# Performance work log

Hardware: AMD Instinct MI355X
Metric: run time of the kernel (lower is better)

The kernel has to match this reference:

```python
import jax, jax.numpy as jnp
import numpy as np

B, S, D, H = 4, 2048, 1024, 16
HD = D // H  # head_length = 64


def setup_inputs() -> dict:
    key = jax.random.key(0)
    ks = jax.random.split(key, 11)
    s = 1.0 / np.sqrt(D)
    return {
        "queries": jax.random.normal(ks[0], (B, S, D), jnp.float32),
        "keys": jax.random.normal(ks[1], (B, S, D), jnp.float32),
        "values": jax.random.normal(ks[2], (B, S, D), jnp.float32),
        "Wq": jax.random.normal(ks[3], (D, D), jnp.float32) * s,
        "bq": jnp.zeros((D,), jnp.float32),
        "Wk": jax.random.normal(ks[4], (D, D), jnp.float32) * s,
        "bk": jnp.zeros((D,), jnp.float32),
        "Wv": jax.random.normal(ks[5], (D, D), jnp.float32) * s,
        "bv": jnp.zeros((D,), jnp.float32),
        "Wo": jax.random.normal(ks[6], (D, D), jnp.float32) * s,
        "bo": jnp.zeros((D,), jnp.float32),
    }


def reference(queries, keys, values, Wq, bq, Wk, bk, Wv, bv, Wo, bo):
    # Linear projections (torch Linear: x @ W^T + b), split into heads -> [B, H, S, HD]
    def proj(x, W, b):
        return (x @ W.T + b).reshape(B, S, H, HD).transpose(0, 2, 1, 3)

    q = proj(queries, Wq, bq)
    k = proj(keys, Wk, bk)
    v = proj(values, Wv, bv)
    # Scaled dot-product attention, scale = 1/sqrt(head_length)
    scores = jnp.einsum("bhsd,bhtd->bhst", q, k) / jnp.sqrt(jnp.float32(HD))
    attn = jax.nn.softmax(scores, axis=-1)
    out = jnp.einsum("bhst,bhtd->bhsd", attn, v)  # [B, H, S, HD]
    out = out.transpose(0, 2, 1, 3).reshape(B, S, D)
    return out @ Wo.T + bo
```

## Files before the change

### kernel.cpp

```cpp
#include <hip/hip_runtime.h>
#include <stdint.h>
#include <stddef.h>

#define B_ 4
#define S_ 2048
#define D_ 1024
#define H_ 16
#define HD_ 64

#define QSCALE 0.18033688f

typedef __bf16 bf16;
typedef __bf16 bf16x8 __attribute__((ext_vector_type(8)));
typedef __bf16 bf16x4 __attribute__((ext_vector_type(4)));
typedef float f32x4 __attribute__((ext_vector_type(4)));
typedef float f32x16 __attribute__((ext_vector_type(16)));
typedef uint32_t u32x4 __attribute__((ext_vector_type(4)));

__device__ __forceinline__ f32x4 mfma16(bf16x8 a, bf16x8 b, f32x4 c) {
  return __builtin_amdgcn_mfma_f32_16x16x32_bf16(a, b, c, 0, 0, 0);
}
__device__ __forceinline__ f32x16 mfma32(bf16x8 a, bf16x8 b, f32x16 c) {
  return __builtin_amdgcn_mfma_f32_32x32x16_bf16(a, b, c, 0, 0, 0);
}

__device__ __forceinline__ float fexp2(float x) {
#if __has_builtin(__builtin_amdgcn_exp2f)
  return __builtin_amdgcn_exp2f(x);
#else
  return exp2f(x);
#endif
}

__device__ __forceinline__ void gload_lds16(const void* g, void* l) {
  __builtin_amdgcn_global_load_lds(
      (__attribute__((address_space(1))) uint32_t*)(uintptr_t)g,
      (__attribute__((address_space(3))) uint32_t*)l, 16, 0, 0);
}

__device__ __forceinline__ uint32_t cvt_pk(float lo, float hi) {
  uint32_t r;
  asm volatile("v_cvt_pk_bf16_f32 %0, %1, %2" : "=v"(r) : "v"(lo), "v"(hi));
  return r;
}

__device__ __forceinline__ void pl_swap(uint32_t& a, uint32_t& b) {
#if __has_builtin(__builtin_amdgcn_permlane32_swap)
  typedef int i32x2_t __attribute__((ext_vector_type(2)));
  i32x2_t r = __builtin_amdgcn_permlane32_swap((int)a, (int)b, false, false);
  a = (uint32_t)r[0];
  b = (uint32_t)r[1];
#else
  uint32_t pa_ = (uint32_t)__shfl_xor((int)a, 32);
  uint32_t pb_ = (uint32_t)__shfl_xor((int)b, 32);
  bool hi_ = (threadIdx.x & 32) != 0;
  uint32_t na = hi_ ? pb_ : a;
  uint32_t nb = hi_ ? b : pa_;
  a = na;
  b = nb;
#endif
}

__device__ __forceinline__ bf16x8 pack4(uint32_t a, uint32_t b, uint32_t c,
                                        uint32_t d) {
  u32x4 v = {a, b, c, d};
  return __builtin_bit_cast(bf16x8, v);
}

__global__ __launch_bounds__(256) void convert_w(
    const float* __restrict__ a, const float* __restrict__ b,
    const float* __restrict__ c, const float* __restrict__ d,
    bf16* __restrict__ out) {
  int i = (blockIdx.x * 256 + threadIdx.x) * 4;
  const float* srcs[4] = {a, b, c, d};
#pragma unroll
  for (int w = 0; w < 4; ++w) {
    f32x4 x = *(const f32x4*)(srcs[w] + i);
    bf16x4 v;
    v[0] = (bf16)x[0]; v[1] = (bf16)x[1]; v[2] = (bf16)x[2]; v[3] = (bf16)x[3];
    *(bf16x4*)(out + (size_t)w * (D_ * D_) + i) = v;
  }
}

__global__ __launch_bounds__(256) void convert_in(const float* __restrict__ in,
                                                  bf16* __restrict__ out) {
  const int n8 = (B_ * S_ * D_) / 8;
  for (int i = blockIdx.x * 256 + threadIdx.x; i < n8; i += gridDim.x * 256) {
    f32x4 x0 = *(const f32x4*)(in + (size_t)i * 8);
    f32x4 x1 = *(const f32x4*)(in + (size_t)i * 8 + 4);
    bf16x8 v;
    v[0] = (bf16)x0[0]; v[1] = (bf16)x0[1]; v[2] = (bf16)x0[2]; v[3] = (bf16)x0[3];
    v[4] = (bf16)x1[0]; v[5] = (bf16)x1[1]; v[6] = (bf16)x1[2]; v[7] = (bf16)x1[3];
    *(bf16x8*)(out + (size_t)i * 8) = v;
  }
}

template <int MODE>
__global__ __launch_bounds__(256, 2) void gemm_bf16(
    const bf16* __restrict__ A, const bf16* __restrict__ Wb,
    const float* __restrict__ bias, void* __restrict__ Out, float oscale) {
  __shared__ alignas(128) char lds[32768];
  const int tid = threadIdx.x;
  const int lane = tid & 63;
  const int wave = tid >> 6;
  const int m0 = blockIdx.x * 128;
  const int n0 = blockIdx.y * 128;
  const int wr = wave >> 1, wc = wave & 1;

  f32x4 acc[4][4] = {};

  for (int kt = 0; kt < 16; ++kt) {
    const int k0 = kt * 64;
#pragma unroll
    for (int j = 0; j < 4; ++j) {
      int slot = j * 256 + tid;
      int row = slot >> 3, kb = slot & 7;
      gload_lds16(A + (size_t)(m0 + row) * D_ + k0 + ((kb ^ (row & 7)) << 3),
                  lds + j * 4096 + wave * 1024);
    }
#pragma unroll
    for (int j = 0; j < 4; ++j) {
      int slot = j * 256 + tid;
      int row = slot >> 3, kb = slot & 7;
      gload_lds16(Wb + (size_t)(n0 + row) * D_ + k0 + ((kb ^ (row & 7)) << 3),
                  lds + 16384 + j * 4096 + wave * 1024);
    }
    __syncthreads();
#pragma unroll
    for (int ks = 0; ks < 2; ++ks) {
      bf16x8 af[4], bfr[4];
#pragma unroll
      for (int f = 0; f < 4; ++f) {
        int ar = wr * 64 + f * 16 + (lane & 15);
        af[f] = *(const bf16x8*)(lds + ar * 128 +
                                 (((ks * 4 + (lane >> 4)) ^ (ar & 7)) << 4));
        int br = wc * 64 + f * 16 + (lane & 15);
        bfr[f] = *(const bf16x8*)(lds + 16384 + br * 128 +
                                  (((ks * 4 + (lane >> 4)) ^ (br & 7)) << 4));
      }
#pragma unroll
      for (int i = 0; i < 4; ++i)
#pragma unroll
        for (int j = 0; j < 4; ++j)
          acc[i][j] = mfma16(af[i], bfr[j], acc[i][j]);
    }
    __syncthreads();
  }

#pragma unroll
  for (int j = 0; j < 4; ++j) {
    const int col = n0 + wc * 64 + j * 16 + (lane & 15);
    const float bv_ = bias[col];
    const int h = col >> 6, hd = col & 63;
#pragma unroll
    for (int i = 0; i < 4; ++i) {
      const int row0 = m0 + wr * 64 + i * 16 + ((lane >> 4) << 2);
      if (MODE == 2) {
        float* O = (float*)Out;
#pragma unroll
        for (int r = 0; r < 4; ++r)
          O[(size_t)(row0 + r) * D_ + col] = acc[i][j][r] + bv_;
      } else if (MODE == 0) {
        bf16* O = (bf16*)Out;
#pragma unroll
        for (int r = 0; r < 4; ++r) {
          int row = row0 + r;
          int b = row >> 11, s = row & (S_ - 1);
          O[(((size_t)(b * H_ + h) * S_ + s) << 6) + hd] =
              (bf16)((acc[i][j][r] + bv_) * oscale);
        }
      } else {
        bf16* O = (bf16*)Out;
        int b = row0 >> 11, s0 = row0 & (S_ - 1);
        bf16x4 pk;
#pragma unroll
        for (int r = 0; r < 4; ++r) pk[r] = (bf16)(acc[i][j][r] + bv_);
        *(bf16x4*)(O + ((size_t)(b * H_ + h) * HD_ + hd) * S_ + s0) = pk;
      }
    }
  }
}

__global__ __launch_bounds__(256, 2) void attn_kernel(
    const bf16* __restrict__ Qh, const bf16* __restrict__ Kh,
    const bf16* __restrict__ Vt, bf16* __restrict__ AO) {
  __shared__ alignas(128) char lds[2][16384];
  const int tid = threadIdx.x, lane = tid & 63, wave = tid >> 6;
  const int hi = lane >> 5, l31 = lane & 31;
  const int bid = blockIdx.x;
  const int bh = bid & 63;
  const int qb = bid >> 6;
  const int q0 = qb * 256 + wave * 64;
  const bf16* Qb = Qh + (size_t)bh * S_ * HD_;
  const bf16* Kb = Kh + (size_t)bh * S_ * HD_;
  const bf16* Vb = Vt + (size_t)bh * HD_ * S_;

  bf16x8 qf[2][4];
#pragma unroll
  for (int qg = 0; qg < 2; ++qg)
#pragma unroll
    for (int ks = 0; ks < 4; ++ks)
      qf[qg][ks] = *(const bf16x8*)(Qb + (size_t)(q0 + qg * 32 + l31) * HD_ +
                                    ks * 16 + hi * 8);

  const bf16* gs[4];
  int lo_[4], ginc[4];
#pragma unroll
  for (int j = 0; j < 4; ++j) {
    int f = j * 4 + wave;
    lo_[j] = f * 1024;
    if (f < 8) {
      gs[j] = Kb + (size_t)((f >> 2) * 32 + l31) * HD_ + (f & 3) * 16 + hi * 8;
      ginc[j] = 64 * HD_;
    } else {
      int g = f - 8;
      gs[j] = Vb + (size_t)((g & 1) * 32 + l31) * S_ + (g >> 1) * 16 + hi * 8;
      ginc[j] = 64;
    }
  }

  f32x16 oacc[2][2] = {};
  float dl[2] = {0.f, 0.f};

#pragma unroll
  for (int j = 0; j < 4; ++j) {
    gload_lds16(gs[j], &lds[0][lo_[j]]);
    gs[j] += ginc[j];
  }
  __syncthreads();

  for (int t = 0; t < 32; ++t) {
    const int cur = t & 1;
    if (t < 31) {
#pragma unroll
      for (int j = 0; j < 4; ++j) {
        gload_lds16(gs[j], &lds[cur ^ 1][lo_[j]]);
        gs[j] += ginc[j];
      }
    }
    const char* kbuf = lds[cur];
    const char* vbuf = lds[cur] + 8192;

    f32x16 s[2][2];
    s[0][0] = (f32x16){}; s[0][1] = (f32x16){};
    s[1][0] = (f32x16){}; s[1][1] = (f32x16){};
    __builtin_amdgcn_s_setprio(1);
#pragma unroll
    for (int kb = 0; kb < 2; ++kb)
#pragma unroll
      for (int ks = 0; ks < 4; ++ks) {
        bf16x8 kf = *(const bf16x8*)(kbuf + (kb * 4 + ks) * 1024 + lane * 16);
        s[kb][0] = mfma32(kf, qf[0][ks], s[kb][0]);
        s[kb][1] = mfma32(kf, qf[1][ks], s[kb][1]);
      }
    __builtin_amdgcn_s_setprio(0);

#pragma unroll
    for (int kb = 0; kb < 2; ++kb) {
      bf16x8 pa[2][2];
#pragma unroll
      for (int qg = 0; qg < 2; ++qg) {
        float e[16];
#pragma unroll
        for (int r = 0; r < 16; ++r) e[r] = fexp2(s[kb][qg][r]);
        {
          float a0 = e[0] + e[1], a1 = e[2] + e[3], a2 = e[4] + e[5],
                a3 = e[6] + e[7], a4 = e[8] + e[9], a5 = e[10] + e[11],
                a6 = e[12] + e[13], a7 = e[14] + e[15];
          float b0 = a0 + a1, b1 = a2 + a3, b2 = a4 + a5, b3 = a6 + a7;
          dl[qg] += (b0 + b1) + (b2 + b3);
        }
        uint32_t w0 = cvt_pk(e[0], e[1]), w1 = cvt_pk(e[2], e[3]),
                 w2 = cvt_pk(e[4], e[5]), w3 = cvt_pk(e[6], e[7]),
                 w4 = cvt_pk(e[8], e[9]), w5 = cvt_pk(e[10], e[11]),
                 w6 = cvt_pk(e[12], e[13]), w7 = cvt_pk(e[14], e[15]);
        pl_swap(w0, w2);
        pl_swap(w1, w3);
        pl_swap(w4, w6);
        pl_swap(w5, w7);
        pa[qg][0] = pack4(w0, w1, w2, w3);
        pa[qg][1] = pack4(w4, w5, w6, w7);
      }
      __builtin_amdgcn_s_setprio(1);
#pragma unroll
      for (int ht = 0; ht < 2; ++ht) {
        bf16x8 vf0 =
            *(const bf16x8*)(vbuf + ((kb * 2 + 0) * 2 + ht) * 1024 + lane * 16);
        oacc[0][ht] = mfma32(pa[0][0], vf0, oacc[0][ht]);
        oacc[1][ht] = mfma32(pa[1][0], vf0, oacc[1][ht]);
        bf16x8 vf1 =
            *(const bf16x8*)(vbuf + ((kb * 2 + 1) * 2 + ht) * 1024 + lane * 16);
        oacc[0][ht] = mfma32(pa[0][1], vf1, oacc[0][ht]);
        oacc[1][ht] = mfma32(pa[1][1], vf1, oacc[1][ht]);
      }
      __builtin_amdgcn_s_setprio(0);
    }
    __syncthreads();
  }

  const int b = bh >> 4, h = bh & 15;
#pragma unroll
  for (int qg = 0; qg < 2; ++qg) {
    float d = dl[qg] + __shfl_xor(dl[qg], 32);
    float rden = 1.0f / d;
#pragma unroll
    for (int r = 0; r < 16; ++r) {
      int qr = (r & 3) + 8 * (r >> 2) + 4 * hi;
      float dr = __shfl(rden, qr);
      size_t base = ((size_t)(b * S_ + q0 + qg * 32 + qr)) * D_ + h * 64;
      AO[base + l31] = (bf16)(oacc[qg][0][r] * dr);
      AO[base + 32 + l31] = (bf16)(oacc[qg][1][r] * dr);
    }
  }
}

extern "C" void kernel_launch(void* const* d_in, const int* in_sizes, int n_in,
                              void* d_out, int out_size, void* d_ws,
                              size_t ws_size, hipStream_t stream) {
  (void)in_sizes; (void)n_in; (void)out_size; (void)ws_size;
  const float* q  = (const float*)d_in[0];
  const float* k  = (const float*)d_in[1];
  const float* v  = (const float*)d_in[2];
  const float* Wq = (const float*)d_in[3];
  const float* bq = (const float*)d_in[4];
  const float* Wk = (const float*)d_in[5];
  const float* bk = (const float*)d_in[6];
  const float* Wv = (const float*)d_in[7];
  const float* bv = (const float*)d_in[8];
  const float* Wo = (const float*)d_in[9];
  const float* bo = (const float*)d_in[10];

  bf16* ws = (bf16*)d_ws;
  const size_t WSZ = (size_t)D_ * D_;
  const size_t TSZ = (size_t)B_ * S_ * D_;
  bf16* Wqb = ws;
  bf16* Wkb = ws + WSZ;
  bf16* Wvb = ws + 2 * WSZ;
  bf16* Wob = ws + 3 * WSZ;
  bf16* Abf = ws + 4 * WSZ;
  bf16* Qh  = Abf + TSZ;
  bf16* Kh  = Qh + TSZ;
  bf16* Vt  = Kh + TSZ;
  bf16* AO  = Abf;

  convert_w<<<dim3(1024), dim3(256), 0, stream>>>(Wq, Wk, Wv, Wo, ws);
  dim3 gg(64, 8), bb(256);
  convert_in<<<dim3(2048), bb, 0, stream>>>(q, Abf);
  gemm_bf16<0><<<gg, bb, 0, stream>>>(Abf, Wqb, bq, Qh, QSCALE);
  convert_in<<<dim3(2048), bb, 0, stream>>>(k, Abf);
  gemm_bf16<0><<<gg, bb, 0, stream>>>(Abf, Wkb, bk, Kh, 1.0f);
  convert_in<<<dim3(2048), bb, 0, stream>>>(v, Abf);
  gemm_bf16<1><<<gg, bb, 0, stream>>>(Abf, Wvb, bv, Vt, 1.0f);
  attn_kernel<<<dim3(512), bb, 0, stream>>>(Qh, Kh, Vt, AO);
  gemm_bf16<2><<<gg, bb, 0, stream>>>(AO, Wob, bo, d_out, 1.0f);
}
```

Before: 197.2 us.

## Triple-buffer K/V tiles in attention with partial vmcnt waits

```diff
diff --git a/kernel.cpp b/kernel.cpp
--- a/kernel.cpp
+++ b/kernel.cpp
@@ -184,7 +184,7 @@
 __global__ __launch_bounds__(256, 2) void attn_kernel(
     const bf16* __restrict__ Qh, const bf16* __restrict__ Kh,
     const bf16* __restrict__ Vt, bf16* __restrict__ AO) {
-  __shared__ alignas(128) char lds[2][16384];
+  __shared__ alignas(128) char lds[49152];
   const int tid = threadIdx.x, lane = tid & 63, wave = tid >> 6;
   const int hi = lane >> 5, l31 = lane & 31;
   const int bid = blockIdx.x;
@@ -202,6 +202,7 @@
     for (int ks = 0; ks < 4; ++ks)
       qf[qg][ks] = *(const bf16x8*)(Qb + (size_t)(q0 + qg * 32 + l31) * HD_ +
                                     ks * 16 + hi * 8);
+  asm volatile("s_waitcnt vmcnt(0)" ::: "memory");
 
   const bf16* gs[4];
   int lo_[4], ginc[4];
@@ -222,24 +223,34 @@
   f32x16 oacc[2][2] = {};
   float dl[2] = {0.f, 0.f};
 
+  char* b0 = lds;
+  char* b1 = lds + 16384;
+  char* b2 = lds + 32768;
+
 #pragma unroll
   for (int j = 0; j < 4; ++j) {
-    gload_lds16(gs[j], &lds[0][lo_[j]]);
+    gload_lds16(gs[j], b0 + lo_[j]);
     gs[j] += ginc[j];
   }
-  __syncthreads();
+#pragma unroll
+  for (int j = 0; j < 4; ++j) {
+    gload_lds16(gs[j], b1 + lo_[j]);
+    gs[j] += ginc[j];
+  }
+  asm volatile("s_waitcnt vmcnt(4)" ::: "memory");
+  __builtin_amdgcn_sched_barrier(0);
+  __builtin_amdgcn_s_barrier();
 
   for (int t = 0; t < 32; ++t) {
-    const int cur = t & 1;
-    if (t < 31) {
+    if (t < 30) {
 #pragma unroll
       for (int j = 0; j < 4; ++j) {
-        gload_lds16(gs[j], &lds[cur ^ 1][lo_[j]]);
+        gload_lds16(gs[j], b2 + lo_[j]);
         gs[j] += ginc[j];
       }
     }
-    const char* kbuf = lds[cur];
-    const char* vbuf = lds[cur] + 8192;
+    const char* kbuf = b0;
+    const char* vbuf = b0 + 8192;
 
     f32x16 s[2][2];
     s[0][0] = (f32x16){}; s[0][1] = (f32x16){};
@@ -267,8 +278,8 @@
           float a0 = e[0] + e[1], a1 = e[2] + e[3], a2 = e[4] + e[5],
                 a3 = e[6] + e[7], a4 = e[8] + e[9], a5 = e[10] + e[11],
                 a6 = e[12] + e[13], a7 = e[14] + e[15];
-          float b0 = a0 + a1, b1 = a2 + a3, b2 = a4 + a5, b3 = a6 + a7;
-          dl[qg] += (b0 + b1) + (b2 + b3);
+          float b0_ = a0 + a1, b1_ = a2 + a3, b2_ = a4 + a5, b3_ = a6 + a7;
+          dl[qg] += (b0_ + b1_) + (b2_ + b3_);
         }
         uint32_t w0 = cvt_pk(e[0], e[1]), w1 = cvt_pk(e[2], e[3]),
                  w2 = cvt_pk(e[4], e[5]), w3 = cvt_pk(e[6], e[7]),
@@ -295,7 +306,14 @@
       }
       __builtin_amdgcn_s_setprio(0);
     }
-    __syncthreads();
+
+    if (t < 30)
+      asm volatile("s_waitcnt vmcnt(4)" ::: "memory");
+    else
+      asm volatile("s_waitcnt vmcnt(0)" ::: "memory");
+    __builtin_amdgcn_sched_barrier(0);
+    __builtin_amdgcn_s_barrier();
+    char* tmp = b0; b0 = b1; b1 = b2; b2 = tmp;
   }
 
   const int b = bh >> 4, h = bh & 15;
```

Measured after the change: 197.6 us. Within noise of the previous version (+0.2%).

## Batch Q/K/V conversion and projections into single launches with grid z

Applied to the files above, without the earlier changes.

```diff
diff --git a/kernel.cpp b/kernel.cpp
--- a/kernel.cpp
+++ b/kernel.cpp
@@ -95,6 +95,24 @@
   }
 }
 
+__global__ __launch_bounds__(256) void convert_in3(
+    const float* __restrict__ a, const float* __restrict__ b,
+    const float* __restrict__ c, bf16* __restrict__ out) {
+  const int n8 = (B_ * S_ * D_) / 8;
+  for (int i = blockIdx.x * 256 + threadIdx.x; i < 3 * n8;
+       i += gridDim.x * 256) {
+    int t = i >> 20;
+    int off = i & (n8 - 1);
+    const float* src = t == 0 ? a : (t == 1 ? b : c);
+    f32x4 x0 = *(const f32x4*)(src + (size_t)off * 8);
+    f32x4 x1 = *(const f32x4*)(src + (size_t)off * 8 + 4);
+    bf16x8 v;
+    v[0] = (bf16)x0[0]; v[1] = (bf16)x0[1]; v[2] = (bf16)x0[2]; v[3] = (bf16)x0[3];
+    v[4] = (bf16)x1[0]; v[5] = (bf16)x1[1]; v[6] = (bf16)x1[2]; v[7] = (bf16)x1[3];
+    *(bf16x8*)(out + (size_t)i * 8) = v;
+  }
+}
+
 template <int MODE>
 __global__ __launch_bounds__(256, 2) void gemm_bf16(
     const bf16* __restrict__ A, const bf16* __restrict__ Wb,
@@ -176,6 +194,91 @@
 #pragma unroll
         for (int r = 0; r < 4; ++r) pk[r] = (bf16)(acc[i][j][r] + bv_);
         *(bf16x4*)(O + ((size_t)(b * H_ + h) * HD_ + hd) * S_ + s0) = pk;
+      }
+    }
+  }
+}
+
+__global__ __launch_bounds__(256, 2) void gemm_qkv3(
+    const bf16* __restrict__ Abase, const bf16* __restrict__ Wbase,
+    const float* __restrict__ bq, const float* __restrict__ bk,
+    const float* __restrict__ bv, bf16* __restrict__ Outbase) {
+  __shared__ alignas(128) char lds[32768];
+  const int tid = threadIdx.x;
+  const int lane = tid & 63;
+  const int wave = tid >> 6;
+  const int m0 = blockIdx.x * 128;
+  const int n0 = blockIdx.y * 128;
+  const int wr = wave >> 1, wc = wave & 1;
+  const int z = blockIdx.z;
+  const bf16* A = Abase + (size_t)z * ((size_t)B_ * S_ * D_);
+  const bf16* Wb = Wbase + (size_t)z * (D_ * D_);
+  const float* bias = z == 0 ? bq : (z == 1 ? bk : bv);
+  bf16* Out = Outbase + (size_t)z * ((size_t)B_ * S_ * D_);
+  const float oscale = (z == 0) ? QSCALE : 1.0f;
+
+  f32x4 acc[4][4] = {};
+
+  for (int kt = 0; kt < 16; ++kt) {
+    const int k0 = kt * 64;
+#pragma unroll
+    for (int j = 0; j < 4; ++j) {
+      int slot = j * 256 + tid;
+      int row = slot >> 3, kb = slot & 7;
+      gload_lds16(A + (size_t)(m0 + row) * D_ + k0 + ((kb ^ (row & 7)) << 3),
+                  lds + j * 4096 + wave * 1024);
+    }
+#pragma unroll
+    for (int j = 0; j < 4; ++j) {
+      int slot = j * 256 + tid;
+      int row = slot >> 3, kb = slot & 7;
+      gload_lds16(Wb + (size_t)(n0 + row) * D_ + k0 + ((kb ^ (row & 7)) << 3),
+                  lds + 16384 + j * 4096 + wave * 1024);
+    }
+    __syncthreads();
+#pragma unroll
+    for (int ks = 0; ks < 2; ++ks) {
+      bf16x8 af[4], bfr[4];
+#pragma unroll
+      for (int f = 0; f < 4; ++f) {
+        int ar = wr * 64 + f * 16 + (lane & 15);
+        af[f] = *(const bf16x8*)(lds + ar * 128 +
+                                 (((ks * 4 + (lane >> 4)) ^ (ar & 7)) << 4));
+        int br = wc * 64 + f * 16 + (lane & 15);
+        bfr[f] = *(const bf16x8*)(lds + 16384 + br * 128 +
+                                  (((ks * 4 + (lane >> 4)) ^ (br & 7)) << 4));
+      }
+#pragma unroll
+      for (int i = 0; i < 4; ++i)
+#pragma unroll
+        for (int j = 0; j < 4; ++j)
+          acc[i][j] = mfma16(af[i], bfr[j], acc[i][j]);
+    }
+    __syncthreads();
+  }
+
+#pragma unroll
+  for (int j = 0; j < 4; ++j) {
+    const int col = n0 + wc * 64 + j * 16 + (lane & 15);
+    const float bv_ = bias[col];
+    const int h = col >> 6, hd = col & 63;
+#pragma unroll
+    for (int i = 0; i < 4; ++i) {
+      const int row0 = m0 + wr * 64 + i * 16 + ((lane >> 4) << 2);
+      if (z != 2) {
+#pragma unroll
+        for (int r = 0; r < 4; ++r) {
+          int row = row0 + r;
+          int b = row >> 11, s = row & (S_ - 1);
+          Out[(((size_t)(b * H_ + h) * S_ + s) << 6) + hd] =
+              (bf16)((acc[i][j][r] + bv_) * oscale);
+        }
+      } else {
+        int b = row0 >> 11, s0 = row0 & (S_ - 1);
+        bf16x4 pk;
+#pragma unroll
+        for (int r = 0; r < 4; ++r) pk[r] = (bf16)(acc[i][j][r] + bv_);
+        *(bf16x4*)(Out + ((size_t)(b * H_ + h) * HD_ + hd) * S_ + s0) = pk;
       }
     }
   }
@@ -221,6 +324,7 @@
 
   f32x16 oacc[2][2] = {};
   float dl[2] = {0.f, 0.f};
+  const f32x16 z16 = {};
 
 #pragma unroll
   for (int j = 0; j < 4; ++j) {
@@ -242,16 +346,19 @@
     const char* vbuf = lds[cur] + 8192;
 
     f32x16 s[2][2];
-    s[0][0] = (f32x16){}; s[0][1] = (f32x16){};
-    s[1][0] = (f32x16){}; s[1][1] = (f32x16){};
     __builtin_amdgcn_s_setprio(1);
 #pragma unroll
     for (int kb = 0; kb < 2; ++kb)
 #pragma unroll
       for (int ks = 0; ks < 4; ++ks) {
         bf16x8 kf = *(const bf16x8*)(kbuf + (kb * 4 + ks) * 1024 + lane * 16);
-        s[kb][0] = mfma32(kf, qf[0][ks], s[kb][0]);
-        s[kb][1] = mfma32(kf, qf[1][ks], s[kb][1]);
+        if (ks == 0) {
+          s[kb][0] = mfma32(kf, qf[0][0], z16);
+          s[kb][1] = mfma32(kf, qf[1][0], z16);
+        } else {
+          s[kb][0] = mfma32(kf, qf[0][ks], s[kb][0]);
+          s[kb][1] = mfma32(kf, qf[1][ks], s[kb][1]);
+        }
       }
     __builtin_amdgcn_s_setprio(0);
 
@@ -267,8 +374,8 @@
           float a0 = e[0] + e[1], a1 = e[2] + e[3], a2 = e[4] + e[5],
                 a3 = e[6] + e[7], a4 = e[8] + e[9], a5 = e[10] + e[11],
                 a6 = e[12] + e[13], a7 = e[14] + e[15];
-          float b0 = a0 + a1, b1 = a2 + a3, b2 = a4 + a5, b3 = a6 + a7;
-          dl[qg] += (b0 + b1) + (b2 + b3);
+          float b0_ = a0 + a1, b1_ = a2 + a3, b2_ = a4 + a5, b3_ = a6 + a7;
+          dl[qg] += (b0_ + b1_) + (b2_ + b3_);
         }
         uint32_t w0 = cvt_pk(e[0], e[1]), w1 = cvt_pk(e[2], e[3]),
                  w2 = cvt_pk(e[4], e[5]), w3 = cvt_pk(e[6], e[7]),
@@ -317,7 +424,7 @@
 extern "C" void kernel_launch(void* const* d_in, const int* in_sizes, int n_in,
                               void* d_out, int out_size, void* d_ws,
                               size_t ws_size, hipStream_t stream) {
-  (void)in_sizes; (void)n_in; (void)out_size; (void)ws_size;
+  (void)in_sizes; (void)n_in; (void)out_size;
   const float* q  = (const float*)d_in[0];
   const float* k  = (const float*)d_in[1];
   const float* v  = (const float*)d_in[2];
@@ -333,24 +440,35 @@
   bf16* ws = (bf16*)d_ws;
   const size_t WSZ = (size_t)D_ * D_;
   const size_t TSZ = (size_t)B_ * S_ * D_;
-  bf16* Wqb = ws;
-  bf16* Wkb = ws + WSZ;
-  bf16* Wvb = ws + 2 * WSZ;
-  bf16* Wob = ws + 3 * WSZ;
-  bf16* Abf = ws + 4 * WSZ;
-  bf16* Qh  = Abf + TSZ;
-  bf16* Kh  = Qh + TSZ;
-  bf16* Vt  = Kh + TSZ;
-  bf16* AO  = Abf;
-
-  convert_w<<<dim3(1024), dim3(256), 0, stream>>>(Wq, Wk, Wv, Wo, ws);
+  bf16* Wqkv = ws;
+  bf16* Wob  = ws + 3 * WSZ;
+
   dim3 gg(64, 8), bb(256);
-  convert_in<<<dim3(2048), bb, 0, stream>>>(q, Abf);
-  gemm_bf16<0><<<gg, bb, 0, stream>>>(Abf, Wqb, bq, Qh, QSCALE);
-  convert_in<<<dim3(2048), bb, 0, stream>>>(k, Abf);
-  gemm_bf16<0><<<gg, bb, 0, stream>>>(Abf, Wkb, bk, Kh, 1.0f);
-  convert_in<<<dim3(2048), bb, 0, stream>>>(v, Abf);
-  gemm_bf16<1><<<gg, bb, 0, stream>>>(Abf, Wvb, bv, Vt, 1.0f);
-  attn_kernel<<<dim3(512), bb, 0, stream>>>(Qh, Kh, Vt, AO);
-  gemm_bf16<2><<<gg, bb, 0, stream>>>(AO, Wob, bo, d_out, 1.0f);
-}
+  convert_w<<<dim3(1024), bb, 0, stream>>>(Wq, Wk, Wv, Wo, ws);
+
+  const size_t need_fused = (4 * WSZ + 6 * TSZ) * sizeof(bf16);
+  if (ws_size >= need_fused) {
+    bf16* Abf3 = ws + 4 * WSZ;
+    bf16* QKV  = Abf3 + 3 * TSZ;
+    bf16* AO   = Abf3;
+    convert_in3<<<dim3(4096), bb, 0, stream>>>(q, k, v, Abf3);
+    gemm_qkv3<<<dim3(64, 8, 3), bb, 0, stream>>>(Abf3, Wqkv, bq, bk, bv, QKV);
+    attn_kernel<<<dim3(512), bb, 0, stream>>>(QKV, QKV + TSZ, QKV + 2 * TSZ,
+                                              AO);
+    gemm_bf16<2><<<gg, bb, 0, stream>>>(AO, Wob, bo, d_out, 1.0f);
+  } else {
+    bf16* Abf = ws + 4 * WSZ;
+    bf16* Qh  = Abf + TSZ;
+    bf16* Kh  = Qh + TSZ;
+    bf16* Vt  = Kh + TSZ;
+    bf16* AO  = Abf;
+    convert_in<<<dim3(2048), bb, 0, stream>>>(q, Abf);
+    gemm_bf16<0><<<gg, bb, 0, stream>>>(Abf, Wqkv, bq, Qh, QSCALE);
+    convert_in<<<dim3(2048), bb, 0, stream>>>(k, Abf);
+    gemm_bf16<0><<<gg, bb, 0, stream>>>(Abf, Wqkv + WSZ, bk, Kh, 1.0f);
+    convert_in<<<dim3(2048), bb, 0, stream>>>(v, Abf);
+    gemm_bf16<1><<<gg, bb, 0, stream>>>(Abf, Wqkv + 2 * WSZ, bv, Vt, 1.0f);
+    attn_kernel<<<dim3(512), bb, 0, stream>>>(Qh, Kh, Vt, AO);
+    gemm_bf16<2><<<gg, bb, 0, stream>>>(AO, Wob, bo, d_out, 1.0f);
+  }
+}
```

Result: faster. 189.4 us (-3.9%).
